# Kernel optimization log

Hardware: AMD Instinct MI355X
Metric: run time of the kernel (lower is better)

Reference implementation:

```python
import jax, jax.numpy as jnp
import numpy as np

N_NODES, N_FEAT, HIDDEN, N_EDGES, N_GRAPHS = 50000, 128, 64, 800000, 64
BN_EPS = 1e-5


def setup_inputs() -> dict:
    key = jax.random.key(0)
    ks = jax.random.split(key, 12)
    x = jax.random.normal(ks[0], (N_NODES, N_FEAT), jnp.float32)
    edge_index = jax.random.randint(ks[1], (2, N_EDGES), 0, N_NODES, jnp.int32)
    batch = jnp.sort(jax.random.randint(ks[2], (N_NODES,), 0, N_GRAPHS, jnp.int32))
    s_in = 1.0 / np.sqrt(N_FEAT)
    s_h = 1.0 / np.sqrt(HIDDEN)
    return {
        "x": x,
        "edge_index": edge_index,
        "batch": batch,
        "W_in": jax.random.normal(ks[3], (HIDDEN, N_FEAT), jnp.float32) * s_in,
        "W1": jax.random.normal(ks[4], (HIDDEN, N_FEAT), jnp.float32) * s_in,
        "b1": jnp.zeros((HIDDEN,), jnp.float32),
        "Ws": jax.random.normal(ks[5], (4, HIDDEN, HIDDEN), jnp.float32) * s_h,
        "bs": jnp.zeros((4, HIDDEN), jnp.float32),
        "bn_gamma": jnp.ones((5, HIDDEN), jnp.float32),
        "bn_beta": jnp.zeros((5, HIDDEN), jnp.float32),
        "bn_mean": jnp.zeros((5, HIDDEN), jnp.float32),
        "bn_var": jnp.ones((5, HIDDEN), jnp.float32),
        "lin_w": jax.random.normal(ks[6], (1, HIDDEN), jnp.float32) * s_h,
        "lin_b": jnp.zeros((1,), jnp.float32),
    }


def reference(x, edge_index, batch, W_in, W1, b1, Ws, bs, bn_gamma, bn_beta, bn_mean, bn_var, lin_w, lin_b):
    N = x.shape[0]
    # add self loops (GCNConv default), symmetric normalization D^-1/2 (A+I) D^-1/2
    loop = jnp.arange(N, dtype=edge_index.dtype)
    src = jnp.concatenate([edge_index[0], loop])  # [E+N]
    dst = jnp.concatenate([edge_index[1], loop])
    deg = jax.ops.segment_sum(jnp.ones_like(dst, jnp.float32), dst, num_segments=N)
    dinv = jax.lax.rsqrt(deg)  # deg >= 1 due to self-loops
    norm = dinv[src] * dinv[dst]  # [E+N]

    def gcn(h, W, b):
        h = h @ W.T                          # [N, H]
        msg = h[src] * norm[:, None]          # gather + edge scaling
        out = jax.ops.segment_sum(msg, dst, num_segments=N)  # scatter-add
        return out + b

    def bn(h, i):
        # eval-mode BatchNorm1d with running stats
        return (h - bn_mean[i]) * (bn_gamma[i] * jax.lax.rsqrt(bn_var[i] + BN_EPS)) + bn_beta[i]

    identity = x @ W_in.T  # input projection for residual
    # layer 1 (dropout = identity in eval)
    h = jax.nn.relu(bn(gcn(x, W1, b1), 0)) + identity
    # layers 2-4 with residual
    for i in range(3):
        h = jax.nn.relu(bn(gcn(h, Ws[i], bs[i]), i + 1)) + h
    # layer 5, no residual afterwards
    h = jax.nn.relu(bn(gcn(h, Ws[3], bs[3]), 4))

    # global mean pool over graphs
    sums = jax.ops.segment_sum(h, batch, num_segments=N_GRAPHS)
    cnts = jax.ops.segment_sum(jnp.ones((N,), jnp.float32), batch, num_segments=N_GRAPHS)
    pooled = sums / jnp.maximum(cnts, 1.0)[:, None]  # [G, H]
    return pooled @ lin_w.T + lin_b  # [G, 1]
```

## Files before the change

kernel.cpp:

```cpp
#include <hip/hip_runtime.h>
#include <hip/hip_fp16.h>

#define N_NODES 50000
#define N_FEAT  128
#define HID     64
#define N_EDGES 800000
#define N_GRAPHS 64
#define MAXDEG  64
#define BN_EPS  1e-5f
#define NB256(n) (((n) + 255) / 256)

__global__ __launch_bounds__(256) void k_zero(int* fill) {
    int i = blockIdx.x * 256 + threadIdx.x;
    if (i < N_NODES) fill[i] = 0;
}

template <int K, bool HOUT>
__device__ __forceinline__ void gemm_body(int vb,
                                          const float* __restrict__ in,
                                          const float* __restrict__ W,
                                          float* __restrict__ outf,
                                          __half* __restrict__ outh,
                                          float4* Wt, float4* xs) {
    constexpr int K4 = K / 4;
    const int t = threadIdx.x;
    const int base = vb * 40;

    const float4* xv = (const float4*)(in + (long long)base * K);
    for (int i = t; i < 40 * K4; i += 256) xs[i] = xv[i];

    const float4* Wv = (const float4*)W;
    const int hh = t & 63;
    const int ng = t >> 6;
    float4 acc[10];
#pragma unroll
    for (int j = 0; j < 10; ++j) acc[j] = make_float4(0.f, 0.f, 0.f, 0.f);

    for (int c = 0; c < K4; c += 16) {
        __syncthreads();
        for (int i = t; i < HID * 16; i += 256) {
            int h2 = i >> 4, k4 = i & 15;
            Wt[k4 * 65 + h2] = Wv[h2 * K4 + c + k4];
        }
        __syncthreads();
#pragma unroll
        for (int k4 = 0; k4 < 16; ++k4) {
            float4 w = Wt[k4 * 65 + hh];
#pragma unroll
            for (int j = 0; j < 10; ++j) {
                float4 x = xs[(ng + 4 * j) * K4 + c + k4];
                acc[j].x += w.x * x.x;
                acc[j].y += w.y * x.y;
                acc[j].z += w.z * x.z;
                acc[j].w += w.w * x.w;
            }
        }
    }
#pragma unroll
    for (int j = 0; j < 10; ++j) {
        int node = base + ng + 4 * j;
        float v = acc[j].x + acc[j].y + acc[j].z + acc[j].w;
        if (HOUT) outh[node * HID + hh] = __float2half(v);
        else      outf[node * HID + hh] = v;
    }
}

#define GE_NB 2500
__global__ __launch_bounds__(256) void k_gemmedge(const int* __restrict__ ei,
                                                  int* fill, unsigned short* __restrict__ colp,
                                                  const float* __restrict__ x,
                                                  const float* __restrict__ W_in,
                                                  const float* __restrict__ W1,
                                                  float* __restrict__ h,
                                                  __half* __restrict__ g16) {
    __shared__ float4 Wt[16 * 65];
    __shared__ float4 xs[40 * 32];
    const int bid = blockIdx.x;
    const int t = threadIdx.x;

    const int ebase = bid * 320;
    int s1 = ei[ebase + t];
    int d1 = ei[N_EDGES + ebase + t];
    int k1 = atomicAdd(&fill[d1], 1);
    int s2 = 0, d2 = 0, k2 = MAXDEG;
    if (t < 64) {
        s2 = ei[ebase + 256 + t];
        d2 = ei[N_EDGES + ebase + 256 + t];
        k2 = atomicAdd(&fill[d2], 1);
    }

    if (bid < 1250)
        gemm_body<N_FEAT, false>(bid, x, W_in, h, nullptr, Wt, xs);
    else
        gemm_body<N_FEAT, true>(bid - 1250, x, W1, nullptr, g16, Wt, xs);

    if (k1 < MAXDEG) colp[d1 * MAXDEG + k1] = (unsigned short)s1;
    if (k2 < MAXDEG) colp[d2 * MAXDEG + k2] = (unsigned short)s2;
}

__device__ __forceinline__ void acc8s(const uint4 r, float* a, float s) {
    float2 f0 = __half22float2(*(const __half2*)&r.x);
    float2 f1 = __half22float2(*(const __half2*)&r.y);
    float2 f2 = __half22float2(*(const __half2*)&r.z);
    float2 f3 = __half22float2(*(const __half2*)&r.w);
    a[0] += s * f0.x; a[1] += s * f0.y; a[2] += s * f1.x; a[3] += s * f1.y;
    a[4] += s * f2.x; a[5] += s * f2.y; a[6] += s * f3.x; a[7] += s * f3.y;
}

template <bool NSCALE, bool DOGEMM>
__global__ __launch_bounds__(256) void k_gather_fused(const __half* __restrict__ gin,
                                                      const unsigned short* __restrict__ colp,
                                                      const int* __restrict__ fill,
                                                      const float* __restrict__ b,
                                                      const float* __restrict__ gamma,
                                                      const float* __restrict__ beta,
                                                      const float* __restrict__ mean,
                                                      const float* __restrict__ var,
                                                      const float4* __restrict__ res4,
                                                      float4* __restrict__ h4,
                                                      const float* __restrict__ W,
                                                      __half* __restrict__ gout) {
    __shared__ float4 Wt[DOGEMM ? 16 * 65 : 1];
    __shared__ float4 hrow[DOGEMM ? 8 * 16 : 1];

    const int t = threadIdx.x;
    const int wv = t >> 6;
    const int lane = t & 63;
    const int hh8 = lane & 7;
    const int sub = lane >> 3;
    const int nA = blockIdx.x * 8 + wv * 2;
    const int nB = nA + 1;

    if (DOGEMM) {
        const float4* Wv = (const float4*)W;
        for (int i = t; i < HID * 16; i += 256) {
            int h2 = i >> 4, k4 = i & 15;
            Wt[k4 * 65 + h2] = Wv[i];
        }
        __syncthreads();
    }

    const uint4* gv = (const uint4*)gin;
    int flA = fill[nA], flB = fill[nB];
    int degA = flA < MAXDEG ? flA : MAXDEG;
    int degB = flB < MAXDEG ? flB : MAXDEG;

    const int myn   = (lane < 32) ? nA : nB;
    const int myj   = lane & 31;
    const int mydeg = (lane < 32) ? degA : degB;
    const bool valid = (myj < mydeg);
    int call = valid ? (int)colp[myn * MAXDEG + myj] : myn;
    float sall;
    if (NSCALE) sall = valid ? rsqrtf((float)fill[call] + 1.0f) : 0.0f;
    else        sall = valid ? 1.0f : 0.0f;

    float aA[8], aB[8];
#pragma unroll
    for (int i = 0; i < 8; ++i) { aA[i] = 0.f; aB[i] = 0.f; }

    int dA32 = degA < 32 ? degA : 32;
    int dB32 = degB < 32 ? degB : 32;
    int nra = (dA32 + 7) >> 3;
    int nrb = (dB32 + 7) >> 3;
    int nr = nra > nrb ? nra : nrb;
#pragma unroll 4
    for (int r = 0; r < nr; ++r) {
        int j = r * 8 + sub;
        if (r < nra) {
            int c = __shfl(call, j);
            float s = __shfl(sall, j);
            acc8s(gv[c * 8 + hh8], aA, s);
        }
        if (r < nrb) {
            int c = __shfl(call, 32 + j);
            float s = __shfl(sall, 32 + j);
            acc8s(gv[c * 8 + hh8], aB, s);
        }
    }
    if (degA > 32) {
        for (int j = 32 + sub; j < degA; j += 8) {
            int c = (int)colp[nA * MAXDEG + j];
            float s = NSCALE ? rsqrtf((float)fill[c] + 1.0f) : 1.0f;
            acc8s(gv[c * 8 + hh8], aA, s);
        }
    }
    if (degB > 32) {
        for (int j = 32 + sub; j < degB; j += 8) {
            int c = (int)colp[nB * MAXDEG + j];
            float s = NSCALE ? rsqrtf((float)fill[c] + 1.0f) : 1.0f;
            acc8s(gv[c * 8 + hh8], aB, s);
        }
    }

#pragma unroll
    for (int m = 8; m <= 32; m <<= 1) {
#pragma unroll
        for (int i = 0; i < 8; ++i) { aA[i] += __shfl_xor(aA[i], m); aB[i] += __shfl_xor(aB[i], m); }
    }

    const float diA = rsqrtf((float)flA + 1.0f);
    const float diB = rsqrtf((float)flB + 1.0f);
    acc8s(gv[nA * 8 + hh8], aA, NSCALE ? diA : 1.0f);
    acc8s(gv[nB * 8 + hh8], aB, NSCALE ? diB : 1.0f);

    float4 b0 = ((const float4*)b)[hh8 * 2],     b1 = ((const float4*)b)[hh8 * 2 + 1];
    float4 g0 = ((const float4*)gamma)[hh8 * 2], g1 = ((const float4*)gamma)[hh8 * 2 + 1];
    float4 e0 = ((const float4*)beta)[hh8 * 2],  e1 = ((const float4*)beta)[hh8 * 2 + 1];
    float4 m0 = ((const float4*)mean)[hh8 * 2],  m1 = ((const float4*)mean)[hh8 * 2 + 1];
    float4 v0 = ((const float4*)var)[hh8 * 2],   v1 = ((const float4*)var)[hh8 * 2 + 1];

    float bb[8] = {b0.x, b0.y, b0.z, b0.w, b1.x, b1.y, b1.z, b1.w};
    float gg[8] = {g0.x, g0.y, g0.z, g0.w, g1.x, g1.y, g1.z, g1.w};
    float ee[8] = {e0.x, e0.y, e0.z, e0.w, e1.x, e1.y, e1.z, e1.w};
    float mm[8] = {m0.x, m0.y, m0.z, m0.w, m1.x, m1.y, m1.z, m1.w};
    float vv[8] = {v0.x, v0.y, v0.z, v0.w, v1.x, v1.y, v1.z, v1.w};

    float oA[8], oB[8];
#pragma unroll
    for (int i = 0; i < 8; ++i) {
        float sc = gg[i] * rsqrtf(vv[i] + BN_EPS);
        float vA = (aA[i] * diA + bb[i] - mm[i]) * sc + ee[i];
        float vB = (aB[i] * diB + bb[i] - mm[i]) * sc + ee[i];
        oA[i] = fmaxf(vA, 0.f);
        oB[i] = fmaxf(vB, 0.f);
    }
    if (res4) {
        float4 rA0 = res4[nA * 16 + hh8 * 2], rA1 = res4[nA * 16 + hh8 * 2 + 1];
        float4 rB0 = res4[nB * 16 + hh8 * 2], rB1 = res4[nB * 16 + hh8 * 2 + 1];
        oA[0] += rA0.x; oA[1] += rA0.y; oA[2] += rA0.z; oA[3] += rA0.w;
        oA[4] += rA1.x; oA[5] += rA1.y; oA[6] += rA1.z; oA[7] += rA1.w;
        oB[0] += rB0.x; oB[1] += rB0.y; oB[2] += rB0.z; oB[3] += rB0.w;
        oB[4] += rB1.x; oB[5] += rB1.y; oB[6] += rB1.z; oB[7] += rB1.w;
    }
    float4 loA = make_float4(oA[0], oA[1], oA[2], oA[3]);
    float4 hiA = make_float4(oA[4], oA[5], oA[6], oA[7]);
    float4 loB = make_float4(oB[0], oB[1], oB[2], oB[3]);
    float4 hiB = make_float4(oB[4], oB[5], oB[6], oB[7]);
    if (sub == 0) {
        h4[nA * 16 + hh8 * 2]     = loA;
        h4[nA * 16 + hh8 * 2 + 1] = hiA;
        h4[nB * 16 + hh8 * 2]     = loB;
        h4[nB * 16 + hh8 * 2 + 1] = hiB;
        if (DOGEMM) {
            hrow[(wv * 2) * 16 + hh8 * 2]         = loA;
            hrow[(wv * 2) * 16 + hh8 * 2 + 1]     = hiA;
            hrow[(wv * 2 + 1) * 16 + hh8 * 2]     = loB;
            hrow[(wv * 2 + 1) * 16 + hh8 * 2 + 1] = hiB;
        }
    }

    if (DOGEMM) {
        const int hh = lane;
        float4 accA = make_float4(0.f, 0.f, 0.f, 0.f);
        float4 accB = make_float4(0.f, 0.f, 0.f, 0.f);
#pragma unroll
        for (int k4 = 0; k4 < 16; ++k4) {
            float4 w = Wt[k4 * 65 + hh];
            float4 hA = hrow[(wv * 2) * 16 + k4];
            float4 hB = hrow[(wv * 2 + 1) * 16 + k4];
            accA.x += hA.x * w.x; accA.y += hA.y * w.y;
            accA.z += hA.z * w.z; accA.w += hA.w * w.w;
            accB.x += hB.x * w.x; accB.y += hB.y * w.y;
            accB.z += hB.z * w.z; accB.w += hB.w * w.w;
        }
        gout[nA * HID + hh] = __float2half((accA.x + accA.y + accA.z + accA.w) * diA);
        gout[nB * HID + hh] = __float2half((accB.x + accB.y + accB.z + accB.w) * diB);
    }
}

__device__ __forceinline__ int lowerb(const int* __restrict__ b, int val) {
    int lo = 0, hi = N_NODES;
    while (lo < hi) {
        int mid = (lo + hi) >> 1;
        if (b[mid] < val) lo = mid + 1; else hi = mid;
    }
    return lo;
}

__global__ __launch_bounds__(1024) void k_poolfinal(const float* __restrict__ h,
                                                    const int* __restrict__ batch,
                                                    const float* __restrict__ lin_w,
                                                    const float* __restrict__ lin_b,
                                                    float* __restrict__ out) {
    __shared__ float red[16][HID];
    int g = blockIdx.x;
    int w = threadIdx.x >> 6;
    int hh = threadIdx.x & 63;
    int start = lowerb(batch, g);
    int end = lowerb(batch, g + 1);
    int len = end - start;
    float acc = 0.f;
    for (int n = start + w; n < end; n += 16) acc += h[n * HID + hh];
    red[w][hh] = acc;
    __syncthreads();
    if (w == 0) {
        float s = 0.f;
#pragma unroll
        for (int i = 0; i < 16; ++i) s += red[i][hh];
        float c = fmaxf((float)len, 1.0f);
        float v = (s / c) * lin_w[hh];
#pragma unroll
        for (int off = 32; off > 0; off >>= 1) v += __shfl_down(v, off);
        if (hh == 0) out[g] = v + lin_b[0];
    }
}

extern "C" void kernel_launch(void* const* d_in, const int* in_sizes, int n_in,
                              void* d_out, int out_size, void* d_ws, size_t ws_size,
                              hipStream_t stream) {
    const float* x     = (const float*)d_in[0];
    const int*   ei    = (const int*)d_in[1];
    const int*   batch = (const int*)d_in[2];
    const float* W_in  = (const float*)d_in[3];
    const float* W1    = (const float*)d_in[4];
    const float* b1    = (const float*)d_in[5];
    const float* Ws    = (const float*)d_in[6];
    const float* bs_   = (const float*)d_in[7];
    const float* bn_g  = (const float*)d_in[8];
    const float* bn_b  = (const float*)d_in[9];
    const float* bn_m  = (const float*)d_in[10];
    const float* bn_v  = (const float*)d_in[11];
    const float* lin_w = (const float*)d_in[12];
    const float* lin_b = (const float*)d_in[13];
    float* out = (float*)d_out;

    char* q = (char*)d_ws;
    int*            fill = (int*)q;             q += (size_t)50048 * 4;
    unsigned short* colp = (unsigned short*)q;  q += (size_t)N_NODES * MAXDEG * 2;
    __half*         g16a = (__half*)q;          q += (size_t)N_NODES * HID * 2;
    __half*         g16b = (__half*)q;          q += (size_t)N_NODES * HID * 2;
    float*          h    = (float*)q;           q += (size_t)N_NODES * HID * 4;

    const int NB_N   = NB256(N_NODES);
    const int NB_GA2 = N_NODES / 8;
    float4* h4 = (float4*)h;

    k_zero<<<NB_N, 256, 0, stream>>>(fill);
    k_gemmedge<<<GE_NB, 256, 0, stream>>>(ei, fill, colp, x, W_in, W1, h, g16a);

    k_gather_fused<true, true><<<NB_GA2, 256, 0, stream>>>(
        g16a, colp, fill, b1, bn_g, bn_b, bn_m, bn_v,
        (const float4*)h, h4, Ws + 0 * HID * HID, g16b);

    k_gather_fused<false, true><<<NB_GA2, 256, 0, stream>>>(
        g16b, colp, fill, bs_ + 0 * HID,
        bn_g + 1 * HID, bn_b + 1 * HID, bn_m + 1 * HID, bn_v + 1 * HID,
        (const float4*)h, h4, Ws + 1 * HID * HID, g16a);

    k_gather_fused<false, true><<<NB_GA2, 256, 0, stream>>>(
        g16a, colp, fill, bs_ + 1 * HID,
        bn_g + 2 * HID, bn_b + 2 * HID, bn_m + 2 * HID, bn_v + 2 * HID,
        (const float4*)h, h4, Ws + 2 * HID * HID, g16b);

    k_gather_fused<false, true><<<NB_GA2, 256, 0, stream>>>(
        g16b, colp, fill, bs_ + 2 * HID,
        bn_g + 3 * HID, bn_b + 3 * HID, bn_m + 3 * HID, bn_v + 3 * HID,
        (const float4*)h, h4, Ws + 3 * HID * HID, g16a);

    k_gather_fused<false, false><<<NB_GA2, 256, 0, stream>>>(
        g16a, colp, fill, bs_ + 3 * HID,
        bn_g + 4 * HID, bn_b + 4 * HID, bn_m + 4 * HID, bn_v + 4 * HID,
        nullptr, h4, nullptr, nullptr);

    k_poolfinal<<<N_GRAPHS, 1024, 0, stream>>>(h, batch, lin_w, lin_b, out);
}
```

Measured before the change: 362.1 us.

## Compute both input projections per block sharing one x tile

```diff
diff --git a/kernel.cpp b/kernel.cpp
--- a/kernel.cpp
+++ b/kernel.cpp
@@ -15,56 +15,6 @@
     if (i < N_NODES) fill[i] = 0;
 }
 
-template <int K, bool HOUT>
-__device__ __forceinline__ void gemm_body(int vb,
-                                          const float* __restrict__ in,
-                                          const float* __restrict__ W,
-                                          float* __restrict__ outf,
-                                          __half* __restrict__ outh,
-                                          float4* Wt, float4* xs) {
-    constexpr int K4 = K / 4;
-    const int t = threadIdx.x;
-    const int base = vb * 40;
-
-    const float4* xv = (const float4*)(in + (long long)base * K);
-    for (int i = t; i < 40 * K4; i += 256) xs[i] = xv[i];
-
-    const float4* Wv = (const float4*)W;
-    const int hh = t & 63;
-    const int ng = t >> 6;
-    float4 acc[10];
-#pragma unroll
-    for (int j = 0; j < 10; ++j) acc[j] = make_float4(0.f, 0.f, 0.f, 0.f);
-
-    for (int c = 0; c < K4; c += 16) {
-        __syncthreads();
-        for (int i = t; i < HID * 16; i += 256) {
-            int h2 = i >> 4, k4 = i & 15;
-            Wt[k4 * 65 + h2] = Wv[h2 * K4 + c + k4];
-        }
-        __syncthreads();
-#pragma unroll
-        for (int k4 = 0; k4 < 16; ++k4) {
-            float4 w = Wt[k4 * 65 + hh];
-#pragma unroll
-            for (int j = 0; j < 10; ++j) {
-                float4 x = xs[(ng + 4 * j) * K4 + c + k4];
-                acc[j].x += w.x * x.x;
-                acc[j].y += w.y * x.y;
-                acc[j].z += w.z * x.z;
-                acc[j].w += w.w * x.w;
-            }
-        }
-    }
-#pragma unroll
-    for (int j = 0; j < 10; ++j) {
-        int node = base + ng + 4 * j;
-        float v = acc[j].x + acc[j].y + acc[j].z + acc[j].w;
-        if (HOUT) outh[node * HID + hh] = __float2half(v);
-        else      outf[node * HID + hh] = v;
-    }
-}
-
 #define GE_NB 2500
 __global__ __launch_bounds__(256) void k_gemmedge(const int* __restrict__ ei,
                                                   int* fill, unsigned short* __restrict__ colp,
@@ -73,8 +23,8 @@
                                                   const float* __restrict__ W1,
                                                   float* __restrict__ h,
                                                   __half* __restrict__ g16) {
-    __shared__ float4 Wt[16 * 65];
-    __shared__ float4 xs[40 * 32];
+    __shared__ float4 Wt[2][8 * 65];
+    __shared__ float4 xs[20 * 32];
     const int bid = blockIdx.x;
     const int t = threadIdx.x;
 
@@ -89,10 +39,49 @@
         k2 = atomicAdd(&fill[d2], 1);
     }
 
-    if (bid < 1250)
-        gemm_body<N_FEAT, false>(bid, x, W_in, h, nullptr, Wt, xs);
-    else
-        gemm_body<N_FEAT, true>(bid - 1250, x, W1, nullptr, g16, Wt, xs);
+    const int base = bid * 20;
+    const float4* xv = (const float4*)(x + (long long)base * N_FEAT);
+    for (int i = t; i < 20 * 32; i += 256) xs[i] = xv[i];
+
+    const float4* W0v = (const float4*)W_in;
+    const float4* W1v = (const float4*)W1;
+    const int hh = t & 63;
+    const int ng = t >> 6;
+    float4 a0[5], a1[5];
+#pragma unroll
+    for (int j = 0; j < 5; ++j) {
+        a0[j] = make_float4(0.f, 0.f, 0.f, 0.f);
+        a1[j] = make_float4(0.f, 0.f, 0.f, 0.f);
+    }
+
+    for (int c = 0; c < 32; c += 8) {
+        __syncthreads();
+        for (int i = t; i < 64 * 8; i += 256) {
+            int h2 = i >> 3, k4 = i & 7;
+            Wt[0][k4 * 65 + h2] = W0v[h2 * 32 + c + k4];
+            Wt[1][k4 * 65 + h2] = W1v[h2 * 32 + c + k4];
+        }
+        __syncthreads();
+#pragma unroll
+        for (int k4 = 0; k4 < 8; ++k4) {
+            float4 w0 = Wt[0][k4 * 65 + hh];
+            float4 w1 = Wt[1][k4 * 65 + hh];
+#pragma unroll
+            for (int j = 0; j < 5; ++j) {
+                float4 xx = xs[(ng + 4 * j) * 32 + c + k4];
+                a0[j].x += w0.x * xx.x; a0[j].y += w0.y * xx.y;
+                a0[j].z += w0.z * xx.z; a0[j].w += w0.w * xx.w;
+                a1[j].x += w1.x * xx.x; a1[j].y += w1.y * xx.y;
+                a1[j].z += w1.z * xx.z; a1[j].w += w1.w * xx.w;
+            }
+        }
+    }
+#pragma unroll
+    for (int j = 0; j < 5; ++j) {
+        int node = base + ng + 4 * j;
+        h[node * HID + hh]   = a0[j].x + a0[j].y + a0[j].z + a0[j].w;
+        g16[node * HID + hh] = __float2half(a1[j].x + a1[j].y + a1[j].z + a1[j].w);
+    }
 
     if (k1 < MAXDEG) colp[d1 * MAXDEG + k1] = (unsigned short)s1;
     if (k2 < MAXDEG) colp[d2 * MAXDEG + k2] = (unsigned short)s2;
```

Measured after the change: 348.9 us. 3.6% less time.
